# Kernel optimization log

Measured on AMD Instinct MI355X. Metric: run time of the kernel, lower is better.

Reference implementation:

```python
import jax, jax.numpy as jnp
import numpy as np

EPS = 1e-6
LN_EPS = 1e-6

def _mlstm_parallel_stabilized(q, k, v, igate_preact, fgate_preact):
    # q,k,v: (B,NH,S,DH); igate_preact,fgate_preact: (B,NH,S,1)
    B, NH, S, DH = q.shape
    log_fg = jax.nn.log_sigmoid(fgate_preact[..., 0])            # (B,NH,S)
    cs = jnp.cumsum(log_fg, axis=-1)                             # (B,NH,S)
    # log decay matrix: entry (i,j) = cumsum_i - cumsum_j, lower-triangular (j<=i)
    fg_mat = cs[..., :, None] - cs[..., None, :]                 # (B,NH,S,S)
    mask = jnp.tril(jnp.ones((S, S), dtype=bool))
    log_D = jnp.where(mask, fg_mat + igate_preact[..., 0][..., None, :], -jnp.inf)
    max_log_D = jnp.max(log_D, axis=-1, keepdims=True)           # (B,NH,S,1)
    D = jnp.exp(log_D - max_log_D)                               # (B,NH,S,S)
    k_scaled = k / jnp.sqrt(jnp.float32(DH)).astype(k.dtype)
    qk = jnp.einsum('bhsd,bhtd->bhst', q, k_scaled)              # (B,NH,S,S)
    C = qk * D
    normalizer = jnp.maximum(jnp.abs(jnp.sum(C, axis=-1, keepdims=True)), jnp.exp(-max_log_D))
    C_norm = C / (normalizer + EPS)
    return jnp.einsum('bhst,bhtd->bhsd', C_norm, v)              # (B,NH,S,DH)

def _multihead_layernorm(x, weight):
    # x: (B,NH,S,DH), weight: (NH,DH); normalize over DH per head, no bias
    mu = jnp.mean(x, axis=-1, keepdims=True)
    var = jnp.mean(jnp.square(x - mu), axis=-1, keepdims=True)
    xn = (x - mu) * jax.lax.rsqrt(var + LN_EPS)
    return xn * weight[None, :, None, :]

def setup_inputs() -> dict:
    key = jax.random.key(0)
    ks = jax.random.split(key, 6)
    B, S, E, NH = 2, 2048, 1024, 8
    q = jax.random.normal(ks[0], (B, S, E), dtype=jnp.float32)
    k = jax.random.normal(ks[1], (B, S, E), dtype=jnp.float32)
    v = jax.random.normal(ks[2], (B, S, E), dtype=jnp.float32)
    igate_kernel = jnp.zeros((3 * E, NH), dtype=jnp.float32)
    igate_bias = 0.1 * jax.random.normal(ks[3], (NH,), dtype=jnp.float32)
    fgate_kernel = jnp.zeros((3 * E, NH), dtype=jnp.float32)
    fgate_bias = jnp.linspace(3.0, 6.0, NH, dtype=jnp.float32)
    outnorm_weight = jnp.ones((NH, E // NH), dtype=jnp.float32)
    return {"q": q, "k": k, "v": v,
            "igate_kernel": igate_kernel, "igate_bias": igate_bias,
            "fgate_kernel": fgate_kernel, "fgate_bias": fgate_bias,
            "outnorm_weight": outnorm_weight}

def reference(q, k, v, igate_kernel, igate_bias, fgate_kernel, fgate_bias, outnorm_weight):
    B, S, E = q.shape
    NH = igate_bias.shape[0]
    qkv = jnp.concatenate([q, k, v], axis=-1)                    # (B,S,3E)
    igate_preact = qkv @ igate_kernel + igate_bias               # (B,S,NH)
    fgate_preact = qkv @ fgate_kernel + fgate_bias               # (B,S,NH)
    qh = q.reshape(B, S, NH, -1).transpose(0, 2, 1, 3)           # (B,NH,S,DH)
    kh = k.reshape(B, S, NH, -1).transpose(0, 2, 1, 3)
    vh = v.reshape(B, S, NH, -1).transpose(0, 2, 1, 3)
    ig = igate_preact.transpose(0, 2, 1)[..., None]              # (B,NH,S,1)
    fg = fgate_preact.transpose(0, 2, 1)[..., None]
    h = _mlstm_parallel_stabilized(qh, kh, vh, ig, fg)           # (B,NH,S,DH)
    h_norm = _multihead_layernorm(h, outnorm_weight)
    return h_norm.transpose(0, 2, 1, 3).reshape(B, S, -1)        # (B,S,E)
```

## Files before the change

kernel.cpp:

```cpp
#include <hip/hip_runtime.h>
#include <math.h>

#define S_LEN 2048
#define E_DIM 1024
#define NHEAD 8
#define DHEAD 128

typedef short bf16x8 __attribute__((ext_vector_type(8)));
typedef float f32x4 __attribute__((ext_vector_type(4)));
typedef unsigned int u32x4 __attribute__((ext_vector_type(4)));
typedef unsigned int u32x2 __attribute__((ext_vector_type(2)));

constexpr float RSQ_DH  = 0.08838834764831843f;
constexpr float LNRSQ   = -2.4260151319598084f;
constexpr float EPS_NORM = 1e-6f;
constexpr float LN_EPS_C = 1e-6f;

__device__ inline unsigned bfpair(float lo, float hi) {
  unsigned a = __builtin_bit_cast(unsigned, lo);
  unsigned b = __builtin_bit_cast(unsigned, hi);
  a = (a + 0x7fffu + ((a >> 16) & 1u)) >> 16;
  b = (b + 0x7fffu + ((b >> 16) & 1u)) >> 16;
  return a | (b << 16);
}

__device__ inline unsigned cvtpk(float lo, float hi) {
  unsigned r;
  asm("v_cvt_pk_bf16_f32 %0, %1, %2" : "=v"(r) : "v"(lo), "v"(hi));
  return r;
}

__device__ inline void gload_lds16(const void* g, void* lds) {
  __builtin_amdgcn_global_load_lds(
      (const __attribute__((address_space(1))) unsigned int*)g,
      (__attribute__((address_space(3))) unsigned int*)lds, 16, 0, 0);
}
__device__ inline void gload_lds4(const void* g, void* lds) {
  __builtin_amdgcn_global_load_lds(
      (const __attribute__((address_space(1))) unsigned int*)g,
      (__attribute__((address_space(3))) unsigned int*)lds, 4, 0, 0);
}

__global__ __launch_bounds__(256) void gates_fused(
    const float* __restrict__ q, const float* __restrict__ k, const float* __restrict__ v,
    const float* __restrict__ Wi, const float* __restrict__ bi,
    const float* __restrict__ Wf, const float* __restrict__ bf,
    float* __restrict__ ig_pre, float* __restrict__ fg_pre,
    unsigned short* __restrict__ kb) {
  const int t = threadIdx.x;
  const int row0 = blockIdx.x * 4;
  const int b = row0 >> 11;
  const int s0 = row0 & 2047;
  float p[4][16];
#pragma unroll
  for (int rr = 0; rr < 4; ++rr)
#pragma unroll
    for (int c = 0; c < 16; ++c) p[rr][c] = 0.f;

#pragma unroll
  for (int i = 0; i < 3; ++i) {
    const float* base = (i == 0) ? q : (i == 1) ? k : v;
    float xs[4][4];
#pragma unroll
    for (int rr = 0; rr < 4; ++rr) {
      const float4 xv = *(const float4*)(base + (size_t)(row0 + rr) * E_DIM + t * 4);
      xs[rr][0] = xv.x; xs[rr][1] = xv.y; xs[rr][2] = xv.z; xs[rr][3] = xv.w;
    }
#pragma unroll
    for (int j = 0; j < 4; ++j) {
      const int ge = i * E_DIM + t * 4 + j;
      const float4 wiA = *(const float4*)(Wi + (size_t)ge * 8);
      const float4 wiB = *(const float4*)(Wi + (size_t)ge * 8 + 4);
      const float4 wfA = *(const float4*)(Wf + (size_t)ge * 8);
      const float4 wfB = *(const float4*)(Wf + (size_t)ge * 8 + 4);
      const float wv16[16] = {wiA.x, wiA.y, wiA.z, wiA.w, wiB.x, wiB.y, wiB.z, wiB.w,
                              wfA.x, wfA.y, wfA.z, wfA.w, wfB.x, wfB.y, wfB.z, wfB.w};
#pragma unroll
      for (int rr = 0; rr < 4; ++rr) {
        const float x = xs[rr][j];
#pragma unroll
        for (int c = 0; c < 16; ++c) p[rr][c] += x * wv16[c];
      }
    }
    if (i == 1 && kb != nullptr) {
      const int h = (t * 4) >> 7, d = (t * 4) & 127;
#pragma unroll
      for (int rr = 0; rr < 4; ++rr) {
        u32x2 pk;
        pk.x = bfpair(xs[rr][0], xs[rr][1]);
        pk.y = bfpair(xs[rr][2], xs[rr][3]);
        *(u32x2*)(kb + (((size_t)b * NHEAD + h) * S_LEN + (s0 + rr)) * DHEAD + d) = pk;
      }
    }
  }

#pragma unroll
  for (int rr = 0; rr < 4; ++rr)
#pragma unroll
    for (int c = 0; c < 16; ++c) {
      float val = p[rr][c];
      val += __shfl_xor(val, 1);
      val += __shfl_xor(val, 2);
      val += __shfl_xor(val, 4);
      val += __shfl_xor(val, 8);
      val += __shfl_xor(val, 16);
      val += __shfl_xor(val, 32);
      p[rr][c] = val;
    }
  __shared__ float sred[4][4][16];
  const int wid = t >> 6, lane = t & 63;
  if (lane == 0) {
#pragma unroll
    for (int rr = 0; rr < 4; ++rr)
#pragma unroll
      for (int c = 0; c < 16; ++c) sred[wid][rr][c] = p[rr][c];
  }
  __syncthreads();
  if (t < 64) {
    const int rr = t >> 4, c = t & 15;
    float sum = sred[0][rr][c] + sred[1][rr][c] + sred[2][rr][c] + sred[3][rr][c];
    const int h = c & 7;
    const int row = row0 + rr;
    const int bb = row / S_LEN, s = row % S_LEN;
    if (c < 8) ig_pre[((size_t)bb * NHEAD + h) * S_LEN + s] = sum + bi[h];
    else       fg_pre[((size_t)bb * NHEAD + h) * S_LEN + s] = sum + bf[h];
  }
}

__global__ __launch_bounds__(256) void vtrans(const float* __restrict__ v,
                                              unsigned short* __restrict__ vtb) {
  __shared__ unsigned int tile[128][36];
  const int bid = blockIdx.x;
  const int bh = bid >> 5, st = bid & 31;
  const int b = bh >> 3, h = bh & 7;
  const int s0 = st * 64;
  const int t = threadIdx.x;
#pragma unroll
  for (int i = 0; i < 4; ++i) {
    const int task = t + 256 * i;
    const int sp = task & 31, dq = task >> 5;
    const float* src = v + ((size_t)b * S_LEN + s0 + 2 * sp) * E_DIM + h * DHEAD + dq * 4;
    const float4 r0 = *(const float4*)(src);
    const float4 r1 = *(const float4*)(src + E_DIM);
    tile[dq * 4 + 0][sp] = bfpair(r0.x, r1.x);
    tile[dq * 4 + 1][sp] = bfpair(r0.y, r1.y);
    tile[dq * 4 + 2][sp] = bfpair(r0.z, r1.z);
    tile[dq * 4 + 3][sp] = bfpair(r0.w, r1.w);
  }
  __syncthreads();
#pragma unroll
  for (int i = 0; i < 2; ++i) {
    const int task = t + 256 * i;
    const int d = task >> 2, c4 = task & 3;
    u32x4 w0, w1;
    w0.x = tile[d][c4 * 8 + 0]; w0.y = tile[d][c4 * 8 + 1];
    w0.z = tile[d][c4 * 8 + 2]; w0.w = tile[d][c4 * 8 + 3];
    w1.x = tile[d][c4 * 8 + 4]; w1.y = tile[d][c4 * 8 + 5];
    w1.z = tile[d][c4 * 8 + 6]; w1.w = tile[d][c4 * 8 + 7];
    unsigned short* dst = vtb + ((size_t)bh * DHEAD + d) * S_LEN + s0 + c4 * 16;
    *(u32x4*)(dst)     = w0;
    *(u32x4*)(dst + 8) = w1;
  }
}

__global__ __launch_bounds__(256) void scan_kernel(
    const float* __restrict__ ig_pre, const float* __restrict__ fg_pre,
    float* __restrict__ cs_out, float* __restrict__ g_out, float* __restrict__ gmax_out,
    float g_add) {
  const int bhh = blockIdx.x;
  const int t = threadIdx.x;
  const int lane = t & 63, wid = t >> 6;
  const size_t base = (size_t)bhh * S_LEN;
  float vals[8];
  float run = 0.f;
#pragma unroll
  for (int i = 0; i < 8; ++i) {
    const float x = fg_pre[base + t * 8 + i];
    const float lf = fminf(x, 0.f) - log1pf(__expf(-fabsf(x)));
    run += lf;
    vals[i] = run;
  }
  float ws = run;
#pragma unroll
  for (int off = 1; off < 64; off <<= 1) {
    const float v = __shfl_up(ws, off);
    if (lane >= off) ws += v;
  }
  __shared__ float wsum[4];
  if (lane == 63) wsum[wid] = ws;
  __syncthreads();
  float wpre = 0.f;
#pragma unroll
  for (int kk = 0; kk < 4; ++kk)
    if (kk < wid) wpre += wsum[kk];
  const float prefix = wpre + (ws - run);

  float g_loc[8], gm_loc[8];
  float lmax = -3.4e38f;
#pragma unroll
  for (int i = 0; i < 8; ++i) {
    const float csv = vals[i] + prefix;
    vals[i] = csv;
    const float gg = ig_pre[base + t * 8 + i] - csv;
    g_loc[i] = gg;
    lmax = fmaxf(lmax, gg);
    gm_loc[i] = lmax;
  }
  float wm = lmax;
#pragma unroll
  for (int off = 1; off < 64; off <<= 1) {
    const float v = __shfl_up(wm, off);
    if (lane >= off) wm = fmaxf(wm, v);
  }
  __shared__ float wmax[4];
  if (lane == 63) wmax[wid] = wm;
  __syncthreads();
  float mpre = -3.4e38f;
#pragma unroll
  for (int kk = 0; kk < 4; ++kk)
    if (kk < wid) mpre = fmaxf(mpre, wmax[kk]);
  float excl = __shfl_up(wm, 1);
  if (lane == 0) excl = -3.4e38f;
  const float pmax = fmaxf(mpre, excl);

#pragma unroll
  for (int i = 0; i < 8; ++i) {
    cs_out[base + t * 8 + i]   = vals[i];
    g_out[base + t * 8 + i]    = g_loc[i] + g_add;
    gmax_out[base + t * 8 + i] = fmaxf(gm_loc[i], pmax);
  }
}

__global__ __launch_bounds__(128) void mlstm_wf(
    const unsigned short* __restrict__ kb, const unsigned short* __restrict__ vtb,
    const float* __restrict__ q,
    const float* __restrict__ cs, const float* __restrict__ garr, const float* __restrict__ gmax,
    const float* __restrict__ wgt, float* __restrict__ out) {
  __shared__ __align__(16) unsigned char smem[2][16384];
  __shared__ float g_sh[2][32];
  __shared__ float den_sh[2][64];

  const int bid = blockIdx.x;
  const int g16 = bid & 15;
  const int gq = bid >> 4;
  const int hh = gq & 15, ss = gq >> 4;
  const int qt = ss * 16 + ((ss & 1) ? (15 - hh) : hh);
  const int bh = 2 * (g16 & 7) + (g16 >> 3);
  const int b = bh >> 3, h = bh & 7;
  const int t = threadIdx.x;
  const int tp = t >> 6;
  const int l = t & 63;
  const int r = l & 15;
  const int qq = l >> 4;
  const size_t bhS = (size_t)bh * S_LEN;

  unsigned char* kteam = &smem[tp][0];
  unsigned char* vteam = &smem[tp][8192];
  float* gteam = &g_sh[tp][0];

  const int grA = qt * 32 + 2 * r;
  const int grB = grA + 1;
  const float gmA = gmax[bhS + grA];
  const float gmB = gmax[bhS + grB];
  const float rAB = __expf(gmA - gmB);

  bf16x8 qfA[4], qfB[4];
  {
    const float* qrowA = q + ((size_t)b * S_LEN + grA) * E_DIM + h * DHEAD;
    const float* qrowB = q + ((size_t)b * S_LEN + grB) * E_DIM + h * DHEAD;
#pragma unroll
    for (int c = 0; c < 4; ++c) {
      float4 f0 = *(const float4*)(qrowA + 32 * c + 8 * qq);
      float4 f1 = *(const float4*)(qrowA + 32 * c + 8 * qq + 4);
      u32x4 u;
      u.x = bfpair(f0.x, f0.y); u.y = bfpair(f0.z, f0.w);
      u.z = bfpair(f1.x, f1.y); u.w = bfpair(f1.z, f1.w);
      qfA[c] = __builtin_bit_cast(bf16x8, u);
      f0 = *(const float4*)(qrowB + 32 * c + 8 * qq);
      f1 = *(const float4*)(qrowB + 32 * c + 8 * qq + 4);
      u.x = bfpair(f0.x, f0.y); u.y = bfpair(f0.z, f0.w);
      u.z = bfpair(f1.x, f1.y); u.w = bfpair(f1.z, f1.w);
      qfB[c] = __builtin_bit_cast(bf16x8, u);
    }
  }

  f32x4 oA[8], oB[8];
#pragma unroll
  for (int n = 0; n < 8; ++n) { oA[n] = (f32x4){0,0,0,0}; oB[n] = (f32x4){0,0,0,0}; }
  float denA = 0.f, denB = 0.f;

  const unsigned short* kt = kb + bhS * DHEAD;
  const unsigned short* vt = vtb + (size_t)bh * DHEAD * S_LEN;

  auto stage = [&](int j0) {
#pragma unroll
    for (int a = 0; a < 8; ++a) {
      const int m = a * 64 + l;
      const int u = m ^ ((m >> 4) & 7);
      gload_lds16(kt + (size_t)(j0 + (u >> 4)) * DHEAD + (u & 15) * 8,
                  kteam + (a * 64) * 16);
    }
#pragma unroll
    for (int a = 0; a < 8; ++a) {
      const int m = a * 64 + l;
      const int u = m ^ ((m >> 3) & 7);
      gload_lds16(vt + (size_t)(u >> 2) * S_LEN + j0 + (u & 3) * 8,
                  vteam + (a * 64) * 16);
    }
    if (l < 32) gload_lds4(garr + bhS + j0 + l, gteam);
  };

  auto body = [&](int j0, bool diag) {
    __builtin_amdgcn_s_setprio(1);
    f32x4 sA0 = {0,0,0,0}, sA1 = {0,0,0,0}, sB0 = {0,0,0,0}, sB1 = {0,0,0,0};
#pragma unroll
    for (int c = 0; c < 4; ++c) {
      const int u0 = ((r)      * 16 + 4 * c + qq) ^ (r & 7);
      const int u1 = ((16 + r) * 16 + 4 * c + qq) ^ (r & 7);
      bf16x8 ka0 = *(const bf16x8*)(kteam + u0 * 16);
      bf16x8 ka1 = *(const bf16x8*)(kteam + u1 * 16);
      sA0 = __builtin_amdgcn_mfma_f32_16x16x32_bf16(ka0, qfA[c], sA0, 0, 0, 0);
      sB0 = __builtin_amdgcn_mfma_f32_16x16x32_bf16(ka0, qfB[c], sB0, 0, 0, 0);
      sA1 = __builtin_amdgcn_mfma_f32_16x16x32_bf16(ka1, qfA[c], sA1, 0, 0, 0);
      sB1 = __builtin_amdgcn_mfma_f32_16x16x32_bf16(ka1, qfB[c], sB1, 0, 0, 0);
    }
    __builtin_amdgcn_s_setprio(0);

    unsigned PA0[2], PA1[2], PB0[2], PB1[2];
    {
      float wa[4], wb[4];
#pragma unroll
      for (int m = 0; m < 4; ++m) {
        const int jl = 4 * qq + m;
        const float e = __expf(gteam[jl] - gmA);
        float a = sA0[m] * e;
        float bq = sB0[m] * e * rAB;
        if (diag) {
          if (j0 + jl > grA) a = 0.f;
          if (j0 + jl > grB) bq = 0.f;
        }
        wa[m] = a; wb[m] = bq; denA += a; denB += bq;
      }
      PA0[0] = cvtpk(wa[0], wa[1]); PA0[1] = cvtpk(wa[2], wa[3]);
      PB0[0] = cvtpk(wb[0], wb[1]); PB0[1] = cvtpk(wb[2], wb[3]);
#pragma unroll
      for (int m = 0; m < 4; ++m) {
        const int jl = 16 + 4 * qq + m;
        const float e = __expf(gteam[jl] - gmA);
        float a = sA1[m] * e;
        float bq = sB1[m] * e * rAB;
        if (diag) {
          if (j0 + jl > grA) a = 0.f;
          if (j0 + jl > grB) bq = 0.f;
        }
        wa[m] = a; wb[m] = bq; denA += a; denB += bq;
      }
      PA1[0] = cvtpk(wa[0], wa[1]); PA1[1] = cvtpk(wa[2], wa[3]);
      PB1[0] = cvtpk(wb[0], wb[1]); PB1[1] = cvtpk(wb[2], wb[3]);
    }

    unsigned AA[4], AB[4];
#pragma unroll
    for (int m = 0; m < 4; ++m) {
      const int srcl = r + 16 * (2 * (qq & 1) + (m >> 1));
      const unsigned a0 = (unsigned)__shfl((int)PA0[m & 1], srcl);
      const unsigned a1 = (unsigned)__shfl((int)PA1[m & 1], srcl);
      const unsigned b0 = (unsigned)__shfl((int)PB0[m & 1], srcl);
      const unsigned b1 = (unsigned)__shfl((int)PB1[m & 1], srcl);
      AA[m] = (qq < 2) ? a0 : a1;
      AB[m] = (qq < 2) ? b0 : b1;
    }
    u32x4 ua, ub;
    ua.x = AA[0]; ua.y = AA[1]; ua.z = AA[2]; ua.w = AA[3];
    ub.x = AB[0]; ub.y = AB[1]; ub.z = AB[2]; ub.w = AB[3];
    const bf16x8 paA = __builtin_bit_cast(bf16x8, ua);
    const bf16x8 paB = __builtin_bit_cast(bf16x8, ub);

    __builtin_amdgcn_s_setprio(1);
#pragma unroll
    for (int n = 0; n < 8; ++n) {
      const int ud = (16 * n + r) * 4 + qq;
      const int up = ud ^ ((ud >> 3) & 7);
      bf16x8 vb = *(const bf16x8*)(vteam + up * 16);
      oA[n] = __builtin_amdgcn_mfma_f32_16x16x32_bf16(paA, vb, oA[n], 0, 0, 0);
      oB[n] = __builtin_amdgcn_mfma_f32_16x16x32_bf16(paB, vb, oB[n], 0, 0, 0);
    }
    __builtin_amdgcn_s_setprio(0);
  };

  const int nt = (qt >= tp) ? ((qt - tp) >> 1) + 1 : 0;
  for (int it = 0; it < nt; ++it) {
    const int jt = 2 * it + tp;
    const int j0 = jt * 32;
    __builtin_amdgcn_sched_barrier(0);
    stage(j0);
    asm volatile("s_waitcnt vmcnt(0)" ::: "memory");
    __builtin_amdgcn_sched_barrier(0);
    body(j0, jt == qt);
    __builtin_amdgcn_sched_barrier(0);
  }

  __syncthreads();
  float* osh = (float*)&smem[0][0];
  if (tp == 1) {
#pragma unroll
    for (int n = 0; n < 8; ++n) {
      const int i0 = (((16 * n + r) * 32 + qq * 8 + 0) ^ ((r & 7) << 2));
      const int i1 = (((16 * n + r) * 32 + qq * 8 + 4) ^ ((r & 7) << 2));
      *(f32x4*)&osh[i0] = oA[n];
      *(f32x4*)&osh[i1] = oB[n];
    }
    den_sh[0][l] = denA;
    den_sh[1][l] = denB;
  }
  __syncthreads();
  if (tp == 0) {
    denA += den_sh[0][l];
    denB += den_sh[1][l];
#pragma unroll
    for (int n = 0; n < 8; ++n) {
      const int i0 = (((16 * n + r) * 32 + qq * 8 + 0) ^ ((r & 7) << 2));
      const int i1 = (((16 * n + r) * 32 + qq * 8 + 4) ^ ((r & 7) << 2));
      oA[n] += *(const f32x4*)&osh[i0];
      oB[n] += *(const f32x4*)&osh[i1];
    }

    const float* wrow = wgt + h * DHEAD;
    float wv_n[8];
#pragma unroll
    for (int n = 0; n < 8; ++n) wv_n[n] = wrow[16 * n + r];

#pragma unroll
    for (int fg = 0; fg < 2; ++fg) {
      float den_f = (fg == 0) ? denA : denB;
      den_f += __shfl_xor(den_f, 16);
      den_f += __shfl_xor(den_f, 32);
#pragma unroll
      for (int m = 0; m < 4; ++m) {
        const int iloc = 4 * qq + m;
        const float den_o = __shfl(den_f, iloc);
        const int grow = qt * 32 + 2 * iloc + fg;
        const float csg = cs[bhS + grow];
        const float gmg = gmax[bhS + grow];
        const float norm = fmaxf(fabsf(den_o), __expf(-(csg + gmg))) + EPS_NORM;
        const float inv = 1.f / norm;
        float hv[8];
        float s1 = 0.f, s2 = 0.f;
#pragma unroll
        for (int n = 0; n < 8; ++n) {
          hv[n] = ((fg == 0) ? oA[n][m] : oB[n][m]) * inv;
          s1 += hv[n]; s2 += hv[n] * hv[n];
        }
        s1 += __shfl_xor(s1, 1); s1 += __shfl_xor(s1, 2);
        s1 += __shfl_xor(s1, 4); s1 += __shfl_xor(s1, 8);
        s2 += __shfl_xor(s2, 1); s2 += __shfl_xor(s2, 2);
        s2 += __shfl_xor(s2, 4); s2 += __shfl_xor(s2, 8);
        const float mu  = s1 * (1.f / 128.f);
        const float var = s2 * (1.f / 128.f) - mu * mu;
        const float rstd = rsqrtf(var + LN_EPS_C);
        float* orow = out + ((size_t)b * S_LEN + grow) * E_DIM + h * DHEAD;
#pragma unroll
        for (int n = 0; n < 8; ++n)
          orow[16 * n + r] = (hv[n] - mu) * rstd * wv_n[n];
      }
    }
  }
}

__global__ __launch_bounds__(256) void mlstm_mfma9(
    const unsigned short* __restrict__ kb, const unsigned short* __restrict__ vtb,
    const float* __restrict__ q,
    const float* __restrict__ cs, const float* __restrict__ garr, const float* __restrict__ gmax,
    const float* __restrict__ wgt, float* __restrict__ out) {
  __shared__ __align__(16) unsigned char kbuf[4][8192];
  __shared__ __align__(16) unsigned char vbuf[4][8192];
  __shared__ float g_sh[4][32];
  __shared__ float den_sh[4][64];

  const int bid = blockIdx.x;
  int qb;
  if (bid < 256) qb = 31 - (bid >> 4);
  else           qb = (bid - 256) >> 4;
  const int g16 = bid & 15;
  const int bh = 2 * (g16 & 7) + (g16 >> 3);
  const int b = bh >> 3, h = bh & 7;
  const int t = threadIdx.x;
  const int w = t >> 6;
  const int iw = w & 1;
  const int tp = w >> 1;
  const int l = t & 63;
  const int r = l & 15;
  const int qq = l >> 4;
  const size_t bhS = (size_t)bh * S_LEN;

  const int grA = qb * 64 + 4 * r + 2 * iw;
  const int grB = grA + 1;
  const float gmA = gmax[bhS + grA];
  const float gmB = gmax[bhS + grB];
  const float rAB = __expf(gmA - gmB);

  bf16x8 qfA[4], qfB[4];
  {
    const float* qrowA = q + ((size_t)b * S_LEN + grA) * E_DIM + h * DHEAD;
    const float* qrowB = q + ((size_t)b * S_LEN + grB) * E_DIM + h * DHEAD;
#pragma unroll
    for (int c = 0; c < 4; ++c) {
      float4 f0 = *(const float4*)(qrowA + 32 * c + 8 * qq);
      float4 f1 = *(const float4*)(qrowA + 32 * c + 8 * qq + 4);
      u32x4 u;
      u.x = bfpair(f0.x, f0.y); u.y = bfpair(f0.z, f0.w);
      u.z = bfpair(f1.x, f1.y); u.w = bfpair(f1.z, f1.w);
      qfA[c] = __builtin_bit_cast(bf16x8, u);
      f0 = *(const float4*)(qrowB + 32 * c + 8 * qq);
      f1 = *(const float4*)(qrowB + 32 * c + 8 * qq + 4);
      u.x = bfpair(f0.x, f0.y); u.y = bfpair(f0.z, f0.w);
      u.z = bfpair(f1.x, f1.y); u.w = bfpair(f1.z, f1.w);
      qfB[c] = __builtin_bit_cast(bf16x8, u);
    }
  }

  f32x4 oA[8], oB[8];
#pragma unroll
  for (int n = 0; n < 8; ++n) { oA[n] = (f32x4){0,0,0,0}; oB[n] = (f32x4){0,0,0,0}; }
  float denA = 0.f, denB = 0.f;

  const unsigned short* kt = kb + bhS * DHEAD;
  const unsigned short* vt = vtb + (size_t)bh * DHEAD * S_LEN;

  auto stage = [&](int pair, int set) {
    const int j0 = pair * 64 + tp * 32;
    const int bi = set * 2 + tp;
#pragma unroll
    for (int a = 0; a < 4; ++a) {
      const int m = iw * 256 + a * 64 + l;
      const int u = m ^ ((m >> 4) & 7);
      gload_lds16(kt + ((size_t)(j0 + (u >> 4))) * DHEAD + (u & 15) * 8,
                  &kbuf[bi][(iw * 256 + a * 64) * 16]);
    }
#pragma unroll
    for (int a = 0; a < 4; ++a) {
      const int m = iw * 256 + a * 64 + l;
      const int u = m ^ ((m >> 3) & 7);
      gload_lds16(vt + (size_t)(u >> 2) * S_LEN + j0 + (u & 3) * 8,
                  &vbuf[bi][(iw * 256 + a * 64) * 16]);
    }
    if (l < 32) gload_lds4(garr + bhS + j0 + l, &g_sh[bi][0]);
  };

  auto body = [&](int j0, int bi, bool diag) {
    __builtin_amdgcn_s_setprio(1);
    f32x4 sA0 = {0,0,0,0}, sA1 = {0,0,0,0}, sB0 = {0,0,0,0}, sB1 = {0,0,0,0};
#pragma unroll
    for (int c = 0; c < 4; ++c) {
      const int u0 = ((r)      * 16 + 4 * c + qq) ^ (r & 7);
      const int u1 = ((16 + r) * 16 + 4 * c + qq) ^ (r & 7);
      bf16x8 ka0 = *(const bf16x8*)&kbuf[bi][u0 * 16];
      bf16x8 ka1 = *(const bf16x8*)&kbuf[bi][u1 * 16];
      sA0 = __builtin_amdgcn_mfma_f32_16x16x32_bf16(ka0, qfA[c], sA0, 0, 0, 0);
      sB0 = __builtin_amdgcn_mfma_f32_16x16x32_bf16(ka0, qfB[c], sB0, 0, 0, 0);
      sA1 = __builtin_amdgcn_mfma_f32_16x16x32_bf16(ka1, qfA[c], sA1, 0, 0, 0);
      sB1 = __builtin_amdgcn_mfma_f32_16x16x32_bf16(ka1, qfB[c], sB1, 0, 0, 0);
    }
    __builtin_amdgcn_s_setprio(0);

    unsigned PA0[2], PA1[2], PB0[2], PB1[2];
    {
      float wa[4], wb[4];
#pragma unroll
      for (int m = 0; m < 4; ++m) {
        const int jl = 4 * qq + m;
        const float e = __expf(g_sh[bi][jl] - gmA);
        float a = sA0[m] * e;
        float bq = sB0[m] * e * rAB;
        if (diag) {
          if (j0 + jl > grA) a = 0.f;
          if (j0 + jl > grB) bq = 0.f;
        }
        wa[m] = a; wb[m] = bq; denA += a; denB += bq;
      }
      PA0[0] = cvtpk(wa[0], wa[1]); PA0[1] = cvtpk(wa[2], wa[3]);
      PB0[0] = cvtpk(wb[0], wb[1]); PB0[1] = cvtpk(wb[2], wb[3]);
#pragma unroll
      for (int m = 0; m < 4; ++m) {
        const int jl = 16 + 4 * qq + m;
        const float e = __expf(g_sh[bi][jl] - gmA);
        float a = sA1[m] * e;
        float bq = sB1[m] * e * rAB;
        if (diag) {
          if (j0 + jl > grA) a = 0.f;
          if (j0 + jl > grB) bq = 0.f;
        }
        wa[m] = a; wb[m] = bq; denA += a; denB += bq;
      }
      PA1[0] = cvtpk(wa[0], wa[1]); PA1[1] = cvtpk(wa[2], wa[3]);
      PB1[0] = cvtpk(wb[0], wb[1]); PB1[1] = cvtpk(wb[2], wb[3]);
    }

    unsigned AA[4], AB[4];
#pragma unroll
    for (int m = 0; m < 4; ++m) {
      const int srcl = r + 16 * (2 * (qq & 1) + (m >> 1));
      const unsigned a0 = (unsigned)__shfl((int)PA0[m & 1], srcl);
      const unsigned a1 = (unsigned)__shfl((int)PA1[m & 1], srcl);
      const unsigned b0 = (unsigned)__shfl((int)PB0[m & 1], srcl);
      const unsigned b1 = (unsigned)__shfl((int)PB1[m & 1], srcl);
      AA[m] = (qq < 2) ? a0 : a1;
      AB[m] = (qq < 2) ? b0 : b1;
    }
    u32x4 ua, ub;
    ua.x = AA[0]; ua.y = AA[1]; ua.z = AA[2]; ua.w = AA[3];
    ub.x = AB[0]; ub.y = AB[1]; ub.z = AB[2]; ub.w = AB[3];
    const bf16x8 paA = __builtin_bit_cast(bf16x8, ua);
    const bf16x8 paB = __builtin_bit_cast(bf16x8, ub);

    __builtin_amdgcn_s_setprio(1);
#pragma unroll
    for (int n = 0; n < 8; ++n) {
      const int ud = (16 * n + r) * 4 + qq;
      const int up = ud ^ ((ud >> 3) & 7);
      bf16x8 vb = *(const bf16x8*)&vbuf[bi][up * 16];
      oA[n] = __builtin_amdgcn_mfma_f32_16x16x32_bf16(paA, vb, oA[n], 0, 0, 0);
      oB[n] = __builtin_amdgcn_mfma_f32_16x16x32_bf16(paB, vb, oB[n], 0, 0, 0);
    }
    __builtin_amdgcn_s_setprio(0);
  };

  stage(0, 0);
  for (int p = 0; p < qb; ++p) {
    stage(p + 1, (p + 1) & 1);
    asm volatile("s_waitcnt vmcnt(9)" ::: "memory");
    __builtin_amdgcn_sched_barrier(0);
    __syncthreads();
    body(p * 64 + tp * 32, (p & 1) * 2 + tp, false);
    __syncthreads();
  }
  asm volatile("s_waitcnt vmcnt(0)" ::: "memory");
  __builtin_amdgcn_sched_barrier(0);
  __syncthreads();
  body(qb * 64 + tp * 32, (qb & 1) * 2 + tp, true);

  float* osh = (float*)&kbuf[0][0];
  __syncthreads();
  const int xsw = (r & 7) << 2;
  if (tp == 1) {
#pragma unroll
    for (int n = 0; n < 8; ++n) {
      const int i0 = ((((16 * n + r) * 2 + iw) * 2 + 0) * 16 + 4 * qq) ^ xsw;
      const int i1 = ((((16 * n + r) * 2 + iw) * 2 + 1) * 16 + 4 * qq) ^ xsw;
      *(f32x4*)&osh[i0] = oA[n];
      *(f32x4*)&osh[i1] = oB[n];
    }
    den_sh[iw * 2 + 0][l] = denA;
    den_sh[iw * 2 + 1][l] = denB;
  }
  __syncthreads();
  if (tp == 0) {
    denA += den_sh[iw * 2 + 0][l];
    denB += den_sh[iw * 2 + 1][l];
#pragma unroll
    for (int n = 0; n < 8; ++n) {
      const int i0 = ((((16 * n + r) * 2 + iw) * 2 + 0) * 16 + 4 * qq) ^ xsw;
      const int i1 = ((((16 * n + r) * 2 + iw) * 2 + 1) * 16 + 4 * qq) ^ xsw;
      oA[n] += *(const f32x4*)&osh[i0];
      oB[n] += *(const f32x4*)&osh[i1];
    }

    const float* wrow = wgt + h * DHEAD;
    float wv_n[8];
#pragma unroll
    for (int n = 0; n < 8; ++n) wv_n[n] = wrow[16 * n + r];

#pragma unroll
    for (int fg = 0; fg < 2; ++fg) {
      float den_f = (fg == 0) ? denA : denB;
      den_f += __shfl_xor(den_f, 16);
      den_f += __shfl_xor(den_f, 32);
#pragma unroll
      for (int m = 0; m < 4; ++m) {
        const int iloc = 4 * qq + m;
        const float den_o = __shfl(den_f, iloc);
        const int grow = qb * 64 + 4 * iloc + 2 * iw + fg;
        const float csg = cs[bhS + grow];
        const float gmg = gmax[bhS + grow];
        const float norm = fmaxf(fabsf(den_o), __expf(-(csg + gmg))) + EPS_NORM;
        const float inv = 1.f / norm;
        float hv[8];
        float s1 = 0.f, s2 = 0.f;
#pragma unroll
        for (int n = 0; n < 8; ++n) {
          hv[n] = ((fg == 0) ? oA[n][m] : oB[n][m]) * inv;
          s1 += hv[n]; s2 += hv[n] * hv[n];
        }
        s1 += __shfl_xor(s1, 1); s1 += __shfl_xor(s1, 2);
        s1 += __shfl_xor(s1, 4); s1 += __shfl_xor(s1, 8);
        s2 += __shfl_xor(s2, 1); s2 += __shfl_xor(s2, 2);
        s2 += __shfl_xor(s2, 4); s2 += __shfl_xor(s2, 8);
        const float mu  = s1 * (1.f / 128.f);
        const float var = s2 * (1.f / 128.f) - mu * mu;
        const float rstd = rsqrtf(var + LN_EPS_C);
        float* orow = out + ((size_t)b * S_LEN + grow) * E_DIM + h * DHEAD;
#pragma unroll
        for (int n = 0; n < 8; ++n)
          orow[16 * n + r] = (hv[n] - mu) * rstd * wv_n[n];
      }
    }
  }
}

extern "C" void kernel_launch(void* const* d_in, const int* in_sizes, int n_in,
                              void* d_out, int out_size, void* d_ws, size_t ws_size,
                              hipStream_t stream) {
  (void)in_sizes; (void)n_in; (void)out_size;
  const float* q   = (const float*)d_in[0];
  const float* k   = (const float*)d_in[1];
  const float* v   = (const float*)d_in[2];
  const float* Wi  = (const float*)d_in[3];
  const float* bi  = (const float*)d_in[4];
  const float* Wf  = (const float*)d_in[5];
  const float* bf  = (const float*)d_in[6];
  const float* wgt = (const float*)d_in[7];
  float* out = (float*)d_out;
  float* ws  = (float*)d_ws;
  const int BNS = 2 * NHEAD * S_LEN;
  float* ig_pre = ws;
  float* fg_pre = ws + (size_t)BNS;
  float* cs     = ws + (size_t)2 * BNS;
  float* gv     = ws + (size_t)3 * BNS;
  float* gmaxs  = ws + (size_t)4 * BNS;
  unsigned short* kb  = (unsigned short*)(ws + (size_t)5 * BNS);
  unsigned short* vtb = kb + (size_t)16 * S_LEN * DHEAD;

  const size_t need = (size_t)5 * BNS * 4 + (size_t)2 * 16 * S_LEN * DHEAD * 2;
  (void)need;

  gates_fused<<<1024, 256, 0, stream>>>(q, k, v, Wi, bi, Wf, bf, ig_pre, fg_pre, kb);
  vtrans<<<512, 256, 0, stream>>>(v, vtb);
  scan_kernel<<<16, 256, 0, stream>>>(ig_pre, fg_pre, cs, gv, gmaxs, LNRSQ);
  if (ws_size >= need) {
    mlstm_wf<<<1024, 128, 0, stream>>>(kb, vtb, q, cs, gv, gmaxs, wgt, out);
  } else {
    mlstm_mfma9<<<512, 256, 0, stream>>>(kb, vtb, q, cs, gv, gmaxs, wgt, out);
  }
}
```

Measured before the change: 108.4 us.

## Pair mirrored query tiles per block and split key tiles across four waves

Replaces the two-wave mlstm_wf kernel with mlstm_pp. Each 256-thread block now processes two query tiles in sequence, x and 63-x, so every block does roughly the same amount of causal work. The key tiles are spread over four waves instead of two, and three waves' partial accumulators are reduced into wave 0 through shared memory before the normalisation and layernorm epilogue. This aims to remove load imbalance from the causal triangle and to put more waves on each tile. In exchange it doubles LDS use per block, halves the grid to 512 blocks, and adds a bigger reduction and extra barriers per phase.

```diff
diff --git a/kernel.cpp b/kernel.cpp
--- a/kernel.cpp
+++ b/kernel.cpp
@@ -231,239 +231,238 @@
   }
 }
 
-__global__ __launch_bounds__(128) void mlstm_wf(
+__global__ __launch_bounds__(256) void mlstm_pp(
     const unsigned short* __restrict__ kb, const unsigned short* __restrict__ vtb,
     const float* __restrict__ q,
     const float* __restrict__ cs, const float* __restrict__ garr, const float* __restrict__ gmax,
     const float* __restrict__ wgt, float* __restrict__ out) {
-  __shared__ __align__(16) unsigned char smem[2][16384];
-  __shared__ float g_sh[2][32];
-  __shared__ float den_sh[2][64];
+  __shared__ __align__(16) unsigned char smem[4][16384];
+  __shared__ float g_sh[4][32];
+  __shared__ float den_sh[3][2][64];
 
   const int bid = blockIdx.x;
   const int g16 = bid & 15;
-  const int gq = bid >> 4;
-  const int hh = gq & 15, ss = gq >> 4;
-  const int qt = ss * 16 + ((ss & 1) ? (15 - hh) : hh);
+  const int x = bid >> 4;
   const int bh = 2 * (g16 & 7) + (g16 >> 3);
   const int b = bh >> 3, h = bh & 7;
   const int t = threadIdx.x;
-  const int tp = t >> 6;
+  const int w = t >> 6;
   const int l = t & 63;
   const int r = l & 15;
   const int qq = l >> 4;
   const size_t bhS = (size_t)bh * S_LEN;
 
-  unsigned char* kteam = &smem[tp][0];
-  unsigned char* vteam = &smem[tp][8192];
-  float* gteam = &g_sh[tp][0];
-
-  const int grA = qt * 32 + 2 * r;
-  const int grB = grA + 1;
-  const float gmA = gmax[bhS + grA];
-  const float gmB = gmax[bhS + grB];
-  const float rAB = __expf(gmA - gmB);
-
-  bf16x8 qfA[4], qfB[4];
-  {
-    const float* qrowA = q + ((size_t)b * S_LEN + grA) * E_DIM + h * DHEAD;
-    const float* qrowB = q + ((size_t)b * S_LEN + grB) * E_DIM + h * DHEAD;
-#pragma unroll
-    for (int c = 0; c < 4; ++c) {
-      float4 f0 = *(const float4*)(qrowA + 32 * c + 8 * qq);
-      float4 f1 = *(const float4*)(qrowA + 32 * c + 8 * qq + 4);
-      u32x4 u;
-      u.x = bfpair(f0.x, f0.y); u.y = bfpair(f0.z, f0.w);
-      u.z = bfpair(f1.x, f1.y); u.w = bfpair(f1.z, f1.w);
-      qfA[c] = __builtin_bit_cast(bf16x8, u);
-      f0 = *(const float4*)(qrowB + 32 * c + 8 * qq);
-      f1 = *(const float4*)(qrowB + 32 * c + 8 * qq + 4);
-      u.x = bfpair(f0.x, f0.y); u.y = bfpair(f0.z, f0.w);
-      u.z = bfpair(f1.x, f1.y); u.w = bfpair(f1.z, f1.w);
-      qfB[c] = __builtin_bit_cast(bf16x8, u);
-    }
-  }
-
-  f32x4 oA[8], oB[8];
-#pragma unroll
-  for (int n = 0; n < 8; ++n) { oA[n] = (f32x4){0,0,0,0}; oB[n] = (f32x4){0,0,0,0}; }
-  float denA = 0.f, denB = 0.f;
+  unsigned char* kteam = &smem[w][0];
+  unsigned char* vteam = &smem[w][8192];
+  float* gteam = &g_sh[w][0];
 
   const unsigned short* kt = kb + bhS * DHEAD;
   const unsigned short* vt = vtb + (size_t)bh * DHEAD * S_LEN;
-
-  auto stage = [&](int j0) {
-#pragma unroll
-    for (int a = 0; a < 8; ++a) {
-      const int m = a * 64 + l;
-      const int u = m ^ ((m >> 4) & 7);
-      gload_lds16(kt + (size_t)(j0 + (u >> 4)) * DHEAD + (u & 15) * 8,
-                  kteam + (a * 64) * 16);
-    }
-#pragma unroll
-    for (int a = 0; a < 8; ++a) {
-      const int m = a * 64 + l;
-      const int u = m ^ ((m >> 3) & 7);
-      gload_lds16(vt + (size_t)(u >> 2) * S_LEN + j0 + (u & 3) * 8,
-                  vteam + (a * 64) * 16);
-    }
-    if (l < 32) gload_lds4(garr + bhS + j0 + l, gteam);
-  };
-
-  auto body = [&](int j0, bool diag) {
-    __builtin_amdgcn_s_setprio(1);
-    f32x4 sA0 = {0,0,0,0}, sA1 = {0,0,0,0}, sB0 = {0,0,0,0}, sB1 = {0,0,0,0};
-#pragma unroll
-    for (int c = 0; c < 4; ++c) {
-      const int u0 = ((r)      * 16 + 4 * c + qq) ^ (r & 7);
-      const int u1 = ((16 + r) * 16 + 4 * c + qq) ^ (r & 7);
-      bf16x8 ka0 = *(const bf16x8*)(kteam + u0 * 16);
-      bf16x8 ka1 = *(const bf16x8*)(kteam + u1 * 16);
-      sA0 = __builtin_amdgcn_mfma_f32_16x16x32_bf16(ka0, qfA[c], sA0, 0, 0, 0);
-      sB0 = __builtin_amdgcn_mfma_f32_16x16x32_bf16(ka0, qfB[c], sB0, 0, 0, 0);
-      sA1 = __builtin_amdgcn_mfma_f32_16x16x32_bf16(ka1, qfA[c], sA1, 0, 0, 0);
-      sB1 = __builtin_amdgcn_mfma_f32_16x16x32_bf16(ka1, qfB[c], sB1, 0, 0, 0);
-    }
-    __builtin_amdgcn_s_setprio(0);
-
-    unsigned PA0[2], PA1[2], PB0[2], PB1[2];
+  const float* wrow = wgt + h * DHEAD;
+  float wv_n[8];
+#pragma unroll
+  for (int n = 0; n < 8; ++n) wv_n[n] = wrow[16 * n + r];
+
+  for (int ph = 0; ph < 2; ++ph) {
+    const int qt = ph ? (63 - x) : x;
+    const int grA = qt * 32 + 2 * r;
+    const int grB = grA + 1;
+    const float gmA = gmax[bhS + grA];
+    const float gmB = gmax[bhS + grB];
+    const float rAB = __expf(gmA - gmB);
+
+    bf16x8 qfA[4], qfB[4];
     {
-      float wa[4], wb[4];
+      const float* qrowA = q + ((size_t)b * S_LEN + grA) * E_DIM + h * DHEAD;
+      const float* qrowB = q + ((size_t)b * S_LEN + grB) * E_DIM + h * DHEAD;
+#pragma unroll
+      for (int c = 0; c < 4; ++c) {
+        float4 f0 = *(const float4*)(qrowA + 32 * c + 8 * qq);
+        float4 f1 = *(const float4*)(qrowA + 32 * c + 8 * qq + 4);
+        u32x4 u;
+        u.x = bfpair(f0.x, f0.y); u.y = bfpair(f0.z, f0.w);
+        u.z = bfpair(f1.x, f1.y); u.w = bfpair(f1.z, f1.w);
+        qfA[c] = __builtin_bit_cast(bf16x8, u);
+        f0 = *(const float4*)(qrowB + 32 * c + 8 * qq);
+        f1 = *(const float4*)(qrowB + 32 * c + 8 * qq + 4);
+        u.x = bfpair(f0.x, f0.y); u.y = bfpair(f0.z, f0.w);
+        u.z = bfpair(f1.x, f1.y); u.w = bfpair(f1.z, f1.w);
+        qfB[c] = __builtin_bit_cast(bf16x8, u);
+      }
+    }
+
+    f32x4 oA[8], oB[8];
+#pragma unroll
+    for (int n = 0; n < 8; ++n) { oA[n] = (f32x4){0,0,0,0}; oB[n] = (f32x4){0,0,0,0}; }
+    float denA = 0.f, denB = 0.f;
+
+    auto stage = [&](int j0) {
+#pragma unroll
+      for (int a = 0; a < 8; ++a) {
+        const int m = a * 64 + l;
+        const int u = m ^ ((m >> 4) & 7);
+        gload_lds16(kt + (size_t)(j0 + (u >> 4)) * DHEAD + (u & 15) * 8,
+                    kteam + (a * 64) * 16);
+      }
+#pragma unroll
+      for (int a = 0; a < 8; ++a) {
+        const int m = a * 64 + l;
+        const int u = m ^ ((m >> 3) & 7);
+        gload_lds16(vt + (size_t)(u >> 2) * S_LEN + j0 + (u & 3) * 8,
+                    vteam + (a * 64) * 16);
+      }
+      if (l < 32) gload_lds4(garr + bhS + j0 + l, gteam);
+    };
+
+    auto body = [&](int j0, bool diag) {
+      __builtin_amdgcn_s_setprio(1);
+      f32x4 sA0 = {0,0,0,0}, sA1 = {0,0,0,0}, sB0 = {0,0,0,0}, sB1 = {0,0,0,0};
+#pragma unroll
+      for (int c = 0; c < 4; ++c) {
+        const int u0 = ((r)      * 16 + 4 * c + qq) ^ (r & 7);
+        const int u1 = ((16 + r) * 16 + 4 * c + qq) ^ (r & 7);
+        bf16x8 ka0 = *(const bf16x8*)(kteam + u0 * 16);
+        bf16x8 ka1 = *(const bf16x8*)(kteam + u1 * 16);
+        sA0 = __builtin_amdgcn_mfma_f32_16x16x32_bf16(ka0, qfA[c], sA0, 0, 0, 0);
+        sB0 = __builtin_amdgcn_mfma_f32_16x16x32_bf16(ka0, qfB[c], sB0, 0, 0, 0);
+        sA1 = __builtin_amdgcn_mfma_f32_16x16x32_bf16(ka1, qfA[c], sA1, 0, 0, 0);
+        sB1 = __builtin_amdgcn_mfma_f32_16x16x32_bf16(ka1, qfB[c], sB1, 0, 0, 0);
+      }
+      __builtin_amdgcn_s_setprio(0);
+
+      unsigned PA0[2], PA1[2], PB0[2], PB1[2];
+      {
+        float wa[4], wb[4];
+#pragma unroll
+        for (int m = 0; m < 4; ++m) {
+          const int jl = 4 * qq + m;
+          const float e = __expf(gteam[jl] - gmA);
+          float a = sA0[m] * e;
+          float bq = sB0[m] * e * rAB;
+          if (diag) {
+            if (j0 + jl > grA) a = 0.f;
+            if (j0 + jl > grB) bq = 0.f;
+          }
+          wa[m] = a; wb[m] = bq; denA += a; denB += bq;
+        }
+        PA0[0] = cvtpk(wa[0], wa[1]); PA0[1] = cvtpk(wa[2], wa[3]);
+        PB0[0] = cvtpk(wb[0], wb[1]); PB0[1] = cvtpk(wb[2], wb[3]);
+#pragma unroll
+        for (int m = 0; m < 4; ++m) {
+          const int jl = 16 + 4 * qq + m;
+          const float e = __expf(gteam[jl] - gmA);
+          float a = sA1[m] * e;
+          float bq = sB1[m] * e * rAB;
+          if (diag) {
+            if (j0 + jl > grA) a = 0.f;
+            if (j0 + jl > grB) bq = 0.f;
+          }
+          wa[m] = a; wb[m] = bq; denA += a; denB += bq;
+        }
+        PA1[0] = cvtpk(wa[0], wa[1]); PA1[1] = cvtpk(wa[2], wa[3]);
+        PB1[0] = cvtpk(wb[0], wb[1]); PB1[1] = cvtpk(wb[2], wb[3]);
+      }
+
+      unsigned AA[4], AB[4];
 #pragma unroll
       for (int m = 0; m < 4; ++m) {
-        const int jl = 4 * qq + m;
-        const float e = __expf(gteam[jl] - gmA);
-        float a = sA0[m] * e;
-        float bq = sB0[m] * e * rAB;
-        if (diag) {
-          if (j0 + jl > grA) a = 0.f;
-          if (j0 + jl > grB) bq = 0.f;
+        const int srcl = r + 16 * (2 * (qq & 1) + (m >> 1));
+        const unsigned a0 = (unsigned)__shfl((int)PA0[m & 1], srcl);
+        const unsigned a1 = (unsigned)__shfl((int)PA1[m & 1], srcl);
+        const unsigned b0 = (unsigned)__shfl((int)PB0[m & 1], srcl);
+        const unsigned b1 = (unsigned)__shfl((int)PB1[m & 1], srcl);
+        AA[m] = (qq < 2) ? a0 : a1;
+        AB[m] = (qq < 2) ? b0 : b1;
+      }
+      u32x4 ua, ub;
+      ua.x = AA[0]; ua.y = AA[1]; ua.z = AA[2]; ua.w = AA[3];
+      ub.x = AB[0]; ub.y = AB[1]; ub.z = AB[2]; ub.w = AB[3];
+      const bf16x8 paA = __builtin_bit_cast(bf16x8, ua);
+      const bf16x8 paB = __builtin_bit_cast(bf16x8, ub);
+
+      __builtin_amdgcn_s_setprio(1);
+#pragma unroll
+      for (int n = 0; n < 8; ++n) {
+        const int ud = (16 * n + r) * 4 + qq;
+        const int up = ud ^ ((ud >> 3) & 7);
+        bf16x8 vb = *(const bf16x8*)(vteam + up * 16);
+        oA[n] = __builtin_amdgcn_mfma_f32_16x16x32_bf16(paA, vb, oA[n], 0, 0, 0);
+        oB[n] = __builtin_amdgcn_mfma_f32_16x16x32_bf16(paB, vb, oB[n], 0, 0, 0);
+      }
+      __builtin_amdgcn_s_setprio(0);
+    };
+
+    for (int i = w; i <= qt; i += 4) {
+      const int j0 = i * 32;
+      __builtin_amdgcn_sched_barrier(0);
+      stage(j0);
+      asm volatile("s_waitcnt vmcnt(0)" ::: "memory");
+      __builtin_amdgcn_sched_barrier(0);
+      body(j0, i == qt);
+      __builtin_amdgcn_sched_barrier(0);
+    }
+
+    __syncthreads();
+    float* part = (float*)&smem[0][0];
+    if (w >= 1) {
+      const int sw = w - 1;
+#pragma unroll
+      for (int n = 0; n < 8; ++n) {
+        *(f32x4*)&part[(((sw * 8 + n) * 2 + 0) * 64 + l) * 4] = oA[n];
+        *(f32x4*)&part[(((sw * 8 + n) * 2 + 1) * 64 + l) * 4] = oB[n];
+      }
+      den_sh[sw][0][l] = denA;
+      den_sh[sw][1][l] = denB;
+    }
+    __syncthreads();
+    if (w == 0) {
+      denA += den_sh[0][0][l] + den_sh[1][0][l] + den_sh[2][0][l];
+      denB += den_sh[0][1][l] + den_sh[1][1][l] + den_sh[2][1][l];
+#pragma unroll
+      for (int n = 0; n < 8; ++n) {
+#pragma unroll
+        for (int sw = 0; sw < 3; ++sw) {
+          oA[n] += *(const f32x4*)&part[(((sw * 8 + n) * 2 + 0) * 64 + l) * 4];
+          oB[n] += *(const f32x4*)&part[(((sw * 8 + n) * 2 + 1) * 64 + l) * 4];
         }
-        wa[m] = a; wb[m] = bq; denA += a; denB += bq;
-      }
-      PA0[0] = cvtpk(wa[0], wa[1]); PA0[1] = cvtpk(wa[2], wa[3]);
-      PB0[0] = cvtpk(wb[0], wb[1]); PB0[1] = cvtpk(wb[2], wb[3]);
-#pragma unroll
-      for (int m = 0; m < 4; ++m) {
-        const int jl = 16 + 4 * qq + m;
-        const float e = __expf(gteam[jl] - gmA);
-        float a = sA1[m] * e;
-        float bq = sB1[m] * e * rAB;
-        if (diag) {
-          if (j0 + jl > grA) a = 0.f;
-          if (j0 + jl > grB) bq = 0.f;
+      }
+
+#pragma unroll
+      for (int fg = 0; fg < 2; ++fg) {
+        float den_f = (fg == 0) ? denA : denB;
+        den_f += __shfl_xor(den_f, 16);
+        den_f += __shfl_xor(den_f, 32);
+#pragma unroll
+        for (int m = 0; m < 4; ++m) {
+          const int iloc = 4 * qq + m;
+          const float den_o = __shfl(den_f, iloc);
+          const int grow = qt * 32 + 2 * iloc + fg;
+          const float csg = cs[bhS + grow];
+          const float gmg = gmax[bhS + grow];
+          const float norm = fmaxf(fabsf(den_o), __expf(-(csg + gmg))) + EPS_NORM;
+          const float inv = 1.f / norm;
+          float hv[8];
+          float s1 = 0.f, s2 = 0.f;
+#pragma unroll
+          for (int n = 0; n < 8; ++n) {
+            hv[n] = ((fg == 0) ? oA[n][m] : oB[n][m]) * inv;
+            s1 += hv[n]; s2 += hv[n] * hv[n];
+          }
+          s1 += __shfl_xor(s1, 1); s1 += __shfl_xor(s1, 2);
+          s1 += __shfl_xor(s1, 4); s1 += __shfl_xor(s1, 8);
+          s2 += __shfl_xor(s2, 1); s2 += __shfl_xor(s2, 2);
+          s2 += __shfl_xor(s2, 4); s2 += __shfl_xor(s2, 8);
+          const float mu  = s1 * (1.f / 128.f);
+          const float var = s2 * (1.f / 128.f) - mu * mu;
+          const float rstd = rsqrtf(var + LN_EPS_C);
+          float* orow = out + ((size_t)b * S_LEN + grow) * E_DIM + h * DHEAD;
+#pragma unroll
+          for (int n = 0; n < 8; ++n)
+            orow[16 * n + r] = (hv[n] - mu) * rstd * wv_n[n];
         }
-        wa[m] = a; wb[m] = bq; denA += a; denB += bq;
-      }
-      PA1[0] = cvtpk(wa[0], wa[1]); PA1[1] = cvtpk(wa[2], wa[3]);
-      PB1[0] = cvtpk(wb[0], wb[1]); PB1[1] = cvtpk(wb[2], wb[3]);
-    }
-
-    unsigned AA[4], AB[4];
-#pragma unroll
-    for (int m = 0; m < 4; ++m) {
-      const int srcl = r + 16 * (2 * (qq & 1) + (m >> 1));
-      const unsigned a0 = (unsigned)__shfl((int)PA0[m & 1], srcl);
-      const unsigned a1 = (unsigned)__shfl((int)PA1[m & 1], srcl);
-      const unsigned b0 = (unsigned)__shfl((int)PB0[m & 1], srcl);
-      const unsigned b1 = (unsigned)__shfl((int)PB1[m & 1], srcl);
-      AA[m] = (qq < 2) ? a0 : a1;
-      AB[m] = (qq < 2) ? b0 : b1;
-    }
-    u32x4 ua, ub;
-    ua.x = AA[0]; ua.y = AA[1]; ua.z = AA[2]; ua.w = AA[3];
-    ub.x = AB[0]; ub.y = AB[1]; ub.z = AB[2]; ub.w = AB[3];
-    const bf16x8 paA = __builtin_bit_cast(bf16x8, ua);
-    const bf16x8 paB = __builtin_bit_cast(bf16x8, ub);
-
-    __builtin_amdgcn_s_setprio(1);
-#pragma unroll
-    for (int n = 0; n < 8; ++n) {
-      const int ud = (16 * n + r) * 4 + qq;
-      const int up = ud ^ ((ud >> 3) & 7);
-      bf16x8 vb = *(const bf16x8*)(vteam + up * 16);
-      oA[n] = __builtin_amdgcn_mfma_f32_16x16x32_bf16(paA, vb, oA[n], 0, 0, 0);
-      oB[n] = __builtin_amdgcn_mfma_f32_16x16x32_bf16(paB, vb, oB[n], 0, 0, 0);
-    }
-    __builtin_amdgcn_s_setprio(0);
-  };
-
-  const int nt = (qt >= tp) ? ((qt - tp) >> 1) + 1 : 0;
-  for (int it = 0; it < nt; ++it) {
-    const int jt = 2 * it + tp;
-    const int j0 = jt * 32;
-    __builtin_amdgcn_sched_barrier(0);
-    stage(j0);
-    asm volatile("s_waitcnt vmcnt(0)" ::: "memory");
-    __builtin_amdgcn_sched_barrier(0);
-    body(j0, jt == qt);
-    __builtin_amdgcn_sched_barrier(0);
-  }
-
-  __syncthreads();
-  float* osh = (float*)&smem[0][0];
-  if (tp == 1) {
-#pragma unroll
-    for (int n = 0; n < 8; ++n) {
-      const int i0 = (((16 * n + r) * 32 + qq * 8 + 0) ^ ((r & 7) << 2));
-      const int i1 = (((16 * n + r) * 32 + qq * 8 + 4) ^ ((r & 7) << 2));
-      *(f32x4*)&osh[i0] = oA[n];
-      *(f32x4*)&osh[i1] = oB[n];
-    }
-    den_sh[0][l] = denA;
-    den_sh[1][l] = denB;
-  }
-  __syncthreads();
-  if (tp == 0) {
-    denA += den_sh[0][l];
-    denB += den_sh[1][l];
-#pragma unroll
-    for (int n = 0; n < 8; ++n) {
-      const int i0 = (((16 * n + r) * 32 + qq * 8 + 0) ^ ((r & 7) << 2));
-      const int i1 = (((16 * n + r) * 32 + qq * 8 + 4) ^ ((r & 7) << 2));
-      oA[n] += *(const f32x4*)&osh[i0];
-      oB[n] += *(const f32x4*)&osh[i1];
-    }
-
-    const float* wrow = wgt + h * DHEAD;
-    float wv_n[8];
-#pragma unroll
-    for (int n = 0; n < 8; ++n) wv_n[n] = wrow[16 * n + r];
-
-#pragma unroll
-    for (int fg = 0; fg < 2; ++fg) {
-      float den_f = (fg == 0) ? denA : denB;
-      den_f += __shfl_xor(den_f, 16);
-      den_f += __shfl_xor(den_f, 32);
-#pragma unroll
-      for (int m = 0; m < 4; ++m) {
-        const int iloc = 4 * qq + m;
-        const float den_o = __shfl(den_f, iloc);
-        const int grow = qt * 32 + 2 * iloc + fg;
-        const float csg = cs[bhS + grow];
-        const float gmg = gmax[bhS + grow];
-        const float norm = fmaxf(fabsf(den_o), __expf(-(csg + gmg))) + EPS_NORM;
-        const float inv = 1.f / norm;
-        float hv[8];
-        float s1 = 0.f, s2 = 0.f;
-#pragma unroll
-        for (int n = 0; n < 8; ++n) {
-          hv[n] = ((fg == 0) ? oA[n][m] : oB[n][m]) * inv;
-          s1 += hv[n]; s2 += hv[n] * hv[n];
-        }
-        s1 += __shfl_xor(s1, 1); s1 += __shfl_xor(s1, 2);
-        s1 += __shfl_xor(s1, 4); s1 += __shfl_xor(s1, 8);
-        s2 += __shfl_xor(s2, 1); s2 += __shfl_xor(s2, 2);
-        s2 += __shfl_xor(s2, 4); s2 += __shfl_xor(s2, 8);
-        const float mu  = s1 * (1.f / 128.f);
-        const float var = s2 * (1.f / 128.f) - mu * mu;
-        const float rstd = rsqrtf(var + LN_EPS_C);
-        float* orow = out + ((size_t)b * S_LEN + grow) * E_DIM + h * DHEAD;
-#pragma unroll
-        for (int n = 0; n < 8; ++n)
-          orow[16 * n + r] = (hv[n] - mu) * rstd * wv_n[n];
-      }
-    }
+      }
+    }
+    __syncthreads();
   }
 }
 
@@ -731,13 +730,12 @@
   unsigned short* vtb = kb + (size_t)16 * S_LEN * DHEAD;
 
   const size_t need = (size_t)5 * BNS * 4 + (size_t)2 * 16 * S_LEN * DHEAD * 2;
-  (void)need;
 
   gates_fused<<<1024, 256, 0, stream>>>(q, k, v, Wi, bi, Wf, bf, ig_pre, fg_pre, kb);
   vtrans<<<512, 256, 0, stream>>>(v, vtb);
   scan_kernel<<<16, 256, 0, stream>>>(ig_pre, fg_pre, cs, gv, gmaxs, LNRSQ);
   if (ws_size >= need) {
-    mlstm_wf<<<1024, 128, 0, stream>>>(kb, vtb, q, cs, gv, gmaxs, wgt, out);
+    mlstm_pp<<<512, 256, 0, stream>>>(kb, vtb, q, cs, gv, gmaxs, wgt, out);
   } else {
     mlstm_mfma9<<<512, 256, 0, stream>>>(kb, vtb, q, cs, gv, gmaxs, wgt, out);
   }
```

After: 120.2 us. 1.11x slower.
